# Optimization experiments

Measured on AMD Instinct MI355X. Metric: run time of the kernel, lower is better.

Reference implementation:

```python
import jax, jax.numpy as jnp
import numpy as np

N, F_IN, F_OUT, HEADS = 4096, 128, 64, 4


def setup_inputs() -> dict:
    key = jax.random.key(0)
    k1, k2, k3, k4, k5 = jax.random.split(key, 5)
    X = jax.random.normal(k1, (N, F_IN), dtype=jnp.float32)
    A = jax.random.randint(k2, (N, N), 0, 2, dtype=jnp.int32)
    # zero the diagonal: the torch loop always prepends the self node, so the
    # adjacency must not also contain it (would duplicate the self term).
    A = A * (1 - jnp.eye(N, dtype=jnp.int32))
    # per-head Linear(F_IN, F_OUT) weights/bias and Linear(2*F_OUT, 1, bias=False)
    W = jax.random.normal(k3, (HEADS, F_OUT, F_IN), dtype=jnp.float32) / np.sqrt(F_IN)
    b = jax.random.normal(k4, (HEADS, F_OUT), dtype=jnp.float32) * 0.02
    att = jax.random.normal(k5, (HEADS, 2 * F_OUT), dtype=jnp.float32) / np.sqrt(2 * F_OUT)
    return {"X": X, "A": A, "W": W, "b": b, "att": att}


def reference(X, A, W, b, att):
    # H[h, n, o] = line_h(X)
    H = jnp.einsum('nf,hof->hno', X, W) + b[:, None, :]
    f_out = W.shape[1]
    a_src, a_dst = att[:, :f_out], att[:, f_out:]
    # score e_ij = leaky_relu(a_src.H_i + a_dst.H_j)
    s = jnp.einsum('hno,ho->hn', H, a_src)  # query-side term (xi_bar expanded)
    d = jnp.einsum('hno,ho->hn', H, a_dst)  # neighbor-side term
    e = jax.nn.leaky_relu(s[:, :, None] + d[:, None, :])  # [H, N, N]
    # neighbor set = {self} U {j : A_ij != 0}
    mask = (A > 0) | jnp.eye(A.shape[0], dtype=bool)
    e = jnp.where(mask[None], e, -jnp.inf)
    alpha = jax.nn.softmax(e, axis=-1)  # segment softmax per node row
    # weighted sum per head, then mean over heads (sum / head in the original)
    out = jnp.einsum('hnm,hmo->no', alpha, H) / W.shape[0]
    return out  # [N, F_OUT]
```

## Files before the change

kernel.cpp:

```cpp
#include <hip/hip_runtime.h>
#include <hip/hip_bf16.h>


#define NN 4096
#define FIN 128
#define FOUT 64
#define NH 4

typedef __attribute__((ext_vector_type(8))) short bf16x8;
typedef __attribute__((ext_vector_type(4))) float f32x4;
typedef __attribute__((ext_vector_type(4))) unsigned int u32x4;

__device__ __forceinline__ unsigned short f32_bf16(float f) {
    unsigned u = __builtin_bit_cast(unsigned, f);
    u += 0x7fffu + ((u >> 16) & 1u);
    return (unsigned short)(u >> 16);
}

__device__ __forceinline__ void gload16(const void* g, void* l) {
    __builtin_amdgcn_global_load_lds(
        (const __attribute__((address_space(1))) unsigned*)g,
        (__attribute__((address_space(3))) unsigned*)l, 16, 0, 0);
}

__global__ __launch_bounds__(256) void pack_bits(
    const int* __restrict__ A, unsigned long long* __restrict__ Abits)
{
    const int row  = blockIdx.x;
    const int lane = threadIdx.x & 63;
    const int wv   = threadIdx.x >> 6;
    const int* arow = A + (size_t)row * NN;
    #pragma unroll 4
    for (int c = 0; c < 16; ++c) {
        const int col = c * 256 + wv * 64 + lane;
        unsigned long long m = __ballot(__builtin_nontemporal_load(&arow[col]) > 0);
        if (lane == 0) Abits[(size_t)row * 64 + c * 4 + wv] = m;
    }
}

__global__ __launch_bounds__(256) void gat_prep(
    const float* __restrict__ X, const float* __restrict__ W,
    const float* __restrict__ b, const float* __restrict__ att,
    unsigned short* __restrict__ HbfT, float* __restrict__ Hrow,
    float* __restrict__ s_out, float* __restrict__ d_out,
    float* __restrict__ es_g, float* __restrict__ es2_g,
    float* __restrict__ ed_g, float* __restrict__ ed2_g)
{
    const int rb = blockIdx.x;
    const int h  = blockIdx.y;
    const int n0 = rb * 32;
    const int t  = threadIdx.x;

    __shared__ float Xl[32][132];
    __shared__ float Wt[128][68];

    for (int g = t; g < 32 * 32; g += 256) {
        int row = g >> 5, c4 = g & 31;
        float4 v = *(const float4*)&X[(size_t)(n0 + row) * FIN + c4 * 4];
        *(float4*)&Xl[row][c4 * 4] = v;
    }
    for (int g = t; g < 64 * 32; g += 256) {
        int o = g >> 5, c4 = g & 31;
        float4 v = *(const float4*)&W[((size_t)h * FOUT + o) * FIN + c4 * 4];
        Wt[c4 * 4 + 0][o] = v.x; Wt[c4 * 4 + 1][o] = v.y;
        Wt[c4 * 4 + 2][o] = v.z; Wt[c4 * 4 + 3][o] = v.w;
    }
    __syncthreads();

    const int rg = t >> 4;
    const int og = t & 15;
    float acc[2][4] = {};

    #pragma unroll 4
    for (int f4 = 0; f4 < 32; ++f4) {
        float xv[2][4], wv[4][4];
        #pragma unroll
        for (int i = 0; i < 2; ++i) {
            float4 tmp = *(const float4*)&Xl[rg * 2 + i][f4 * 4];
            xv[i][0] = tmp.x; xv[i][1] = tmp.y; xv[i][2] = tmp.z; xv[i][3] = tmp.w;
        }
        #pragma unroll
        for (int k = 0; k < 4; ++k) {
            float4 tmp = *(const float4*)&Wt[f4 * 4 + k][og * 4];
            wv[k][0] = tmp.x; wv[k][1] = tmp.y; wv[k][2] = tmp.z; wv[k][3] = tmp.w;
        }
        #pragma unroll
        for (int i = 0; i < 2; ++i)
            #pragma unroll
            for (int k = 0; k < 4; ++k)
                #pragma unroll
                for (int jj = 0; jj < 4; ++jj)
                    acc[i][jj] = fmaf(xv[i][k], wv[k][jj], acc[i][jj]);
    }

    float bb[4], as_[4], ad_[4];
    #pragma unroll
    for (int jj = 0; jj < 4; ++jj) {
        bb[jj]  = b[h * FOUT + og * 4 + jj];
        as_[jj] = att[h * 2 * FOUT + og * 4 + jj];
        ad_[jj] = att[h * 2 * FOUT + FOUT + og * 4 + jj];
    }
    #pragma unroll
    for (int i = 0; i < 2; ++i)
        #pragma unroll
        for (int jj = 0; jj < 4; ++jj)
            acc[i][jj] += bb[jj];

    float sp[2] = {0.f, 0.f}, dp[2] = {0.f, 0.f};
    #pragma unroll
    for (int i = 0; i < 2; ++i)
        #pragma unroll
        for (int jj = 0; jj < 4; ++jj) {
            sp[i] = fmaf(acc[i][jj], as_[jj], sp[i]);
            dp[i] = fmaf(acc[i][jj], ad_[jj], dp[i]);
        }
    #pragma unroll
    for (int off = 1; off < 16; off <<= 1) {
        #pragma unroll
        for (int i = 0; i < 2; ++i) {
            sp[i] += __shfl_xor(sp[i], off);
            dp[i] += __shfl_xor(dp[i], off);
        }
    }
    if (og == 0) {
        #pragma unroll
        for (int i = 0; i < 2; ++i) {
            int nn = n0 + rg * 2 + i;
            s_out[h * NN + nn]  = sp[i];
            d_out[h * NN + nn]  = dp[i];
            es_g [h * NN + nn]  = __expf(sp[i]);
            es2_g[h * NN + nn]  = __expf(0.01f * sp[i]);
            ed_g [h * NN + nn]  = __expf(dp[i]);
            ed2_g[h * NN + nn]  = __expf(0.01f * dp[i]);
        }
    }

    #pragma unroll
    for (int i = 0; i < 2; ++i) {
        float4 v = make_float4(acc[i][0], acc[i][1], acc[i][2], acc[i][3]);
        *(float4*)&Hrow[((size_t)h * NN + n0 + rg * 2 + i) * FOUT + og * 4] = v;
    }
    #pragma unroll
    for (int jj = 0; jj < 4; ++jj) {
        int o = og * 4 + jj;
        ushort2 p;
        p.x = f32_bf16(acc[0][jj]);
        p.y = f32_bf16(acc[1][jj]);
        *(ushort2*)&HbfT[((size_t)h * FOUT + o) * NN + n0 + rg * 2] = p;
    }
}

struct SMem {
    union {
        __align__(16) unsigned short H[2][64][256];
        struct {
            float red[7][2][16][68];
            float redl[7][2][16];
        } fin;
    };
    unsigned bits[2][32][8];
    float ed [2][256];
    float ed2[2][256];
};

__global__ __launch_bounds__(1024, 8) void gat_main(
    const unsigned* __restrict__ Abits, const unsigned short* __restrict__ HbfT,
    const float* __restrict__ s_g, const float* __restrict__ d_g,
    const float* __restrict__ es_g, const float* __restrict__ es2_g,
    const float* __restrict__ ed_g, const float* __restrict__ ed2_g,
    const float* __restrict__ Hrow, float* __restrict__ outH)
{
    const int id   = blockIdx.x;
    const int h    = id & 3;
    const int tile = id >> 2;
    const int n0   = tile * 32;
    const int tid  = threadIdx.x;
    const int w    = tid >> 6;
    const int lane = tid & 63;
    const int r    = lane & 15;
    const int q    = lane >> 4;
    const int qs   = q * 8;
    const int rg   = w & 1;
    const int kg   = w >> 1;

    __shared__ SMem sm;

    const int nrow = n0 + rg * 16 + r;
    const float es  = es_g [h * NN + nrow];
    const float es2 = es2_g[h * NN + nrow];

    const int cb   = kg * 4 + q;
    const int sblk = (((cb & 15) ^ r) | (cb & 16));

    const int rowA = 4 * w + (lane >> 5);
    const int rowB = rowA + 2;
    const int blk  = lane & 31;
    const int gbA  = (((blk & 15) ^ (rowA & 15)) | (blk & 16));
    const int gbB  = (((blk & 15) ^ (rowB & 15)) | (blk & 16));
    const unsigned short* gHA = HbfT + ((size_t)(h * FOUT) + rowA) * NN + gbA * 8;
    const unsigned short* gHB = HbfT + ((size_t)(h * FOUT) + rowB) * NN + gbB * 8;
    const unsigned* gBits = Abits + (size_t)(n0 + (lane >> 1)) * 128 + (lane & 1) * 4;
    const float* gEd  = ed_g  + (size_t)h * NN + lane * 4;
    const float* gEd2 = ed2_g + (size_t)h * NN + lane * 4;

    bf16x8 ones;
    #pragma unroll
    for (int i = 0; i < 8; ++i) ones[i] = (short)0x3F80;

    f32x4 acc0 = {0,0,0,0}, acc1 = {0,0,0,0}, acc2 = {0,0,0,0},
          acc3 = {0,0,0,0}, accl = {0,0,0,0};

    gload16(gHA, &sm.H[0][4 * w][0]);
    gload16(gHB, &sm.H[0][4 * w + 2][0]);
    if      (w == 0) gload16(gBits, &sm.bits[0][0][0]);
    else if (w == 1) gload16(gEd,   &sm.ed [0][0]);
    else if (w == 2) gload16(gEd2,  &sm.ed2[0][0]);
    __syncthreads();

    #pragma unroll 2
    for (int ch = 0; ch < 16; ++ch) {
        const int buf = ch & 1;

        if (ch < 15) {
            const int nb = buf ^ 1;
            gload16(gHA + (ch + 1) * 256, &sm.H[nb][4 * w][0]);
            gload16(gHB + (ch + 1) * 256, &sm.H[nb][4 * w + 2][0]);
            if      (w == 0) gload16(gBits + (ch + 1) * 8,   &sm.bits[nb][0][0]);
            else if (w == 1) gload16(gEd   + (ch + 1) * 256, &sm.ed [nb][0]);
            else if (w == 2) gload16(gEd2  + (ch + 1) * 256, &sm.ed2[nb][0]);
        }

        const unsigned bits8 = sm.bits[buf][rg * 16 + r][kg] >> qs;
        const float4 e0 = *(const float4*)&sm.ed [buf][kg * 32 + qs];
        const float4 e1 = *(const float4*)&sm.ed [buf][kg * 32 + qs + 4];
        const float4 g0 = *(const float4*)&sm.ed2[buf][kg * 32 + qs];
        const float4 g1 = *(const float4*)&sm.ed2[buf][kg * 32 + qs + 4];
        const float edv [8] = {e0.x, e0.y, e0.z, e0.w, e1.x, e1.y, e1.z, e1.w};
        const float ed2v[8] = {g0.x, g0.y, g0.z, g0.w, g1.x, g1.y, g1.z, g1.w};

        u32x4 afu;
        #pragma unroll
        for (int p = 0; p < 4; ++p) {
            const int j0 = 2 * p, j1 = 2 * p + 1;
            float wa = (bits8 & (1u << j0))
                     ? fmaxf(es * edv[j0], es2 * ed2v[j0]) : 0.0f;
            float wb = (bits8 & (1u << j1))
                     ? fmaxf(es * edv[j1], es2 * ed2v[j1]) : 0.0f;
            __hip_bfloat162 pk = __float22bfloat162_rn(make_float2(wa, wb));
            unsigned u;
            __builtin_memcpy(&u, &pk, sizeof(u));
            afu[p] = u;
        }
        const bf16x8 af = __builtin_bit_cast(bf16x8, afu);

        const bf16x8 b0 = *(const bf16x8*)&sm.H[buf][r     ][sblk * 8];
        const bf16x8 b1 = *(const bf16x8*)&sm.H[buf][r + 16][sblk * 8];
        const bf16x8 b2 = *(const bf16x8*)&sm.H[buf][r + 32][sblk * 8];
        const bf16x8 b3 = *(const bf16x8*)&sm.H[buf][r + 48][sblk * 8];

        acc0 = __builtin_amdgcn_mfma_f32_16x16x32_bf16(af, b0,   acc0, 0, 0, 0);
        acc1 = __builtin_amdgcn_mfma_f32_16x16x32_bf16(af, b1,   acc1, 0, 0, 0);
        acc2 = __builtin_amdgcn_mfma_f32_16x16x32_bf16(af, b2,   acc2, 0, 0, 0);
        acc3 = __builtin_amdgcn_mfma_f32_16x16x32_bf16(af, b3,   acc3, 0, 0, 0);
        accl = __builtin_amdgcn_mfma_f32_16x16x32_bf16(af, ones, accl, 0, 0, 0);

        __syncthreads();
    }

    if (kg > 0) {
        #pragma unroll
        for (int reg = 0; reg < 4; ++reg) {
            const int rr = q * 4 + reg;
            sm.fin.red[kg - 1][rg][rr][ 0 + r] = acc0[reg];
            sm.fin.red[kg - 1][rg][rr][16 + r] = acc1[reg];
            sm.fin.red[kg - 1][rg][rr][32 + r] = acc2[reg];
            sm.fin.red[kg - 1][rg][rr][48 + r] = acc3[reg];
        }
        if (r == 0) {
            #pragma unroll
            for (int reg = 0; reg < 4; ++reg)
                sm.fin.redl[kg - 1][rg][q * 4 + reg] = accl[reg];
        }
    }
    __syncthreads();
    if (kg == 0) {
        #pragma unroll
        for (int kk = 0; kk < 7; ++kk) {
            #pragma unroll
            for (int reg = 0; reg < 4; ++reg) {
                const int rr = q * 4 + reg;
                acc0[reg] += sm.fin.red[kk][rg][rr][ 0 + r];
                acc1[reg] += sm.fin.red[kk][rg][rr][16 + r];
                acc2[reg] += sm.fin.red[kk][rg][rr][32 + r];
                acc3[reg] += sm.fin.red[kk][rg][rr][48 + r];
                accl[reg] += sm.fin.redl[kk][rg][rr];
            }
        }
        #pragma unroll
        for (int reg = 0; reg < 4; ++reg) {
            const int rr  = q * 4 + reg;
            const int nn2 = n0 + rg * 16 + rr;
            const float tt = s_g[h * NN + nn2] + d_g[h * NN + nn2];
            const float wd = __expf(fmaxf(tt, 0.01f * tt));
            const float inv = 0.25f / (accl[reg] + wd);
            const float* hr = &Hrow[((size_t)h * NN + nn2) * FOUT];
            float*       ob = &outH[((size_t)h * NN + nn2) * FOUT];
            ob[ 0 + r] = (acc0[reg] + wd * hr[ 0 + r]) * inv;
            ob[16 + r] = (acc1[reg] + wd * hr[16 + r]) * inv;
            ob[32 + r] = (acc2[reg] + wd * hr[32 + r]) * inv;
            ob[48 + r] = (acc3[reg] + wd * hr[48 + r]) * inv;
        }
    }
}

__global__ __launch_bounds__(256) void gat_fin(
    const float* __restrict__ outH, float* __restrict__ out)
{
    const int i = blockIdx.x * 256 + threadIdx.x;
    const f32x4* p = (const f32x4*)outH;
    f32x4 v0 = __builtin_nontemporal_load(p + i);
    f32x4 v1 = __builtin_nontemporal_load(p + i +  65536);
    f32x4 v2 = __builtin_nontemporal_load(p + i + 131072);
    f32x4 v3 = __builtin_nontemporal_load(p + i + 196608);
    f32x4 s = (v0 + v1) + (v2 + v3);
    *((f32x4*)out + i) = s;
}

extern "C" void kernel_launch(void* const* d_in, const int* in_sizes, int n_in,
                              void* d_out, int out_size, void* d_ws, size_t ws_size,
                              hipStream_t stream) {
    const float* X   = (const float*)d_in[0];
    const int*   A   = (const int*)  d_in[1];
    const float* W   = (const float*)d_in[2];
    const float* b   = (const float*)d_in[3];
    const float* att = (const float*)d_in[4];
    float* out = (float*)d_out;

    char* ws = (char*)d_ws;
    unsigned short* HbfT = (unsigned short*)ws;
    size_t off = (size_t)NH * FOUT * NN * 2;
    float* s_buf   = (float*)(ws + off);  off += (size_t)NH * NN * 4;
    float* d_buf   = (float*)(ws + off);  off += (size_t)NH * NN * 4;
    float* es_buf  = (float*)(ws + off);  off += (size_t)NH * NN * 4;
    float* es2_buf = (float*)(ws + off);  off += (size_t)NH * NN * 4;
    float* ed_buf  = (float*)(ws + off);  off += (size_t)NH * NN * 4;
    float* ed2_buf = (float*)(ws + off);  off += (size_t)NH * NN * 4;
    unsigned long long* Abits = (unsigned long long*)(ws + off);
    off += (size_t)NN * 64 * 8;
    float* Hrow   = (float*)(ws + off);
    off += (size_t)NH * NN * FOUT * 4;
    float* outH   = (float*)(ws + off);
    off += (size_t)NH * NN * FOUT * 4;

    pack_bits<<<NN, 256, 0, stream>>>(A, Abits);
    gat_prep<<<dim3(128, 4), 256, 0, stream>>>(X, W, b, att, HbfT, Hrow,
                                               s_buf, d_buf,
                                               es_buf, es2_buf, ed_buf, ed2_buf);
    gat_main<<<512, 1024, 0, stream>>>((const unsigned*)Abits, HbfT,
                                       s_buf, d_buf,
                                       es_buf, es2_buf, ed_buf, ed2_buf,
                                       Hrow, outH);
    gat_fin<<<256, 256, 0, stream>>>(outH, out);
}
```

Measured before the change: 172.2 us.

## Halve gat_main block to 512 threads, each wave covering two K sub-chunks

Shrinks the main aggregation block from 16 to 8 waves. Each wave now processes two 32-column slices of every 256-column chunk and issues four H tile loads instead of two. The cross-wave reduction shrinks from 7 partial buffers per row group to 3, and fewer waves share each barrier. In exchange, each wave carries more serial MFMA work per chunk, and there are fewer resident waves to hide the async load latency.

```diff
diff --git a/kernel.cpp b/kernel.cpp
--- a/kernel.cpp
+++ b/kernel.cpp
@@ -154,8 +154,8 @@
     union {
         __align__(16) unsigned short H[2][64][256];
         struct {
-            float red[7][2][16][68];
-            float redl[7][2][16];
+            float red[6][16][68];
+            float redl[6][16];
         } fin;
     };
     unsigned bits[2][32][8];
@@ -163,7 +163,7 @@
     float ed2[2][256];
 };
 
-__global__ __launch_bounds__(1024, 8) void gat_main(
+__global__ __launch_bounds__(512, 4) void gat_main(
     const unsigned* __restrict__ Abits, const unsigned short* __restrict__ HbfT,
     const float* __restrict__ s_g, const float* __restrict__ d_g,
     const float* __restrict__ es_g, const float* __restrict__ es2_g,
@@ -189,16 +189,16 @@
     const float es  = es_g [h * NN + nrow];
     const float es2 = es2_g[h * NN + nrow];
 
-    const int cb   = kg * 4 + q;
-    const int sblk = (((cb & 15) ^ r) | (cb & 16));
-
-    const int rowA = 4 * w + (lane >> 5);
-    const int rowB = rowA + 2;
-    const int blk  = lane & 31;
-    const int gbA  = (((blk & 15) ^ (rowA & 15)) | (blk & 16));
-    const int gbB  = (((blk & 15) ^ (rowB & 15)) | (blk & 16));
-    const unsigned short* gHA = HbfT + ((size_t)(h * FOUT) + rowA) * NN + gbA * 8;
-    const unsigned short* gHB = HbfT + ((size_t)(h * FOUT) + rowB) * NN + gbB * 8;
+    const int bb = ((kg * 4 + q) ^ r) & 15;
+
+    const int blk = lane & 31;
+    const unsigned short* gH[4];
+    #pragma unroll
+    for (int i = 0; i < 4; ++i) {
+        const int row = 8 * w + 2 * i + (lane >> 5);
+        const int gb  = ((blk & 15) ^ (row & 15)) | (blk & 16);
+        gH[i] = HbfT + ((size_t)(h * FOUT) + row) * NN + gb * 8;
+    }
     const unsigned* gBits = Abits + (size_t)(n0 + (lane >> 1)) * 128 + (lane & 1) * 4;
     const float* gEd  = ed_g  + (size_t)h * NN + lane * 4;
     const float* gEd2 = ed2_g + (size_t)h * NN + lane * 4;
@@ -210,11 +210,16 @@
     f32x4 acc0 = {0,0,0,0}, acc1 = {0,0,0,0}, acc2 = {0,0,0,0},
           acc3 = {0,0,0,0}, accl = {0,0,0,0};
 
-    gload16(gHA, &sm.H[0][4 * w][0]);
-    gload16(gHB, &sm.H[0][4 * w + 2][0]);
-    if      (w == 0) gload16(gBits, &sm.bits[0][0][0]);
-    else if (w == 1) gload16(gEd,   &sm.ed [0][0]);
-    else if (w == 2) gload16(gEd2,  &sm.ed2[0][0]);
+    {
+        unsigned short* hw = &sm.H[0][8 * w][0];
+        gload16(gH[0], hw);
+        gload16(gH[1], hw +  512);
+        gload16(gH[2], hw + 1024);
+        gload16(gH[3], hw + 1536);
+        if      (w == 0) gload16(gBits, &sm.bits[0][0][0]);
+        else if (w == 1) gload16(gEd,   &sm.ed [0][0]);
+        else if (w == 2) gload16(gEd2,  &sm.ed2[0][0]);
+    }
     __syncthreads();
 
     #pragma unroll 2
@@ -222,78 +227,120 @@
         const int buf = ch & 1;
 
         if (ch < 15) {
-            const int nb = buf ^ 1;
-            gload16(gHA + (ch + 1) * 256, &sm.H[nb][4 * w][0]);
-            gload16(gHB + (ch + 1) * 256, &sm.H[nb][4 * w + 2][0]);
-            if      (w == 0) gload16(gBits + (ch + 1) * 8,   &sm.bits[nb][0][0]);
-            else if (w == 1) gload16(gEd   + (ch + 1) * 256, &sm.ed [nb][0]);
-            else if (w == 2) gload16(gEd2  + (ch + 1) * 256, &sm.ed2[nb][0]);
-        }
-
-        const unsigned bits8 = sm.bits[buf][rg * 16 + r][kg] >> qs;
-        const float4 e0 = *(const float4*)&sm.ed [buf][kg * 32 + qs];
-        const float4 e1 = *(const float4*)&sm.ed [buf][kg * 32 + qs + 4];
-        const float4 g0 = *(const float4*)&sm.ed2[buf][kg * 32 + qs];
-        const float4 g1 = *(const float4*)&sm.ed2[buf][kg * 32 + qs + 4];
-        const float edv [8] = {e0.x, e0.y, e0.z, e0.w, e1.x, e1.y, e1.z, e1.w};
-        const float ed2v[8] = {g0.x, g0.y, g0.z, g0.w, g1.x, g1.y, g1.z, g1.w};
-
-        u32x4 afu;
-        #pragma unroll
-        for (int p = 0; p < 4; ++p) {
-            const int j0 = 2 * p, j1 = 2 * p + 1;
-            float wa = (bits8 & (1u << j0))
-                     ? fmaxf(es * edv[j0], es2 * ed2v[j0]) : 0.0f;
-            float wb = (bits8 & (1u << j1))
-                     ? fmaxf(es * edv[j1], es2 * ed2v[j1]) : 0.0f;
-            __hip_bfloat162 pk = __float22bfloat162_rn(make_float2(wa, wb));
-            unsigned u;
-            __builtin_memcpy(&u, &pk, sizeof(u));
-            afu[p] = u;
-        }
-        const bf16x8 af = __builtin_bit_cast(bf16x8, afu);
-
-        const bf16x8 b0 = *(const bf16x8*)&sm.H[buf][r     ][sblk * 8];
-        const bf16x8 b1 = *(const bf16x8*)&sm.H[buf][r + 16][sblk * 8];
-        const bf16x8 b2 = *(const bf16x8*)&sm.H[buf][r + 32][sblk * 8];
-        const bf16x8 b3 = *(const bf16x8*)&sm.H[buf][r + 48][sblk * 8];
-
-        acc0 = __builtin_amdgcn_mfma_f32_16x16x32_bf16(af, b0,   acc0, 0, 0, 0);
-        acc1 = __builtin_amdgcn_mfma_f32_16x16x32_bf16(af, b1,   acc1, 0, 0, 0);
-        acc2 = __builtin_amdgcn_mfma_f32_16x16x32_bf16(af, b2,   acc2, 0, 0, 0);
-        acc3 = __builtin_amdgcn_mfma_f32_16x16x32_bf16(af, b3,   acc3, 0, 0, 0);
-        accl = __builtin_amdgcn_mfma_f32_16x16x32_bf16(af, ones, accl, 0, 0, 0);
+            const int nb   = buf ^ 1;
+            const int coff = (ch + 1) * 256;
+            unsigned short* hw = &sm.H[nb][8 * w][0];
+            gload16(gH[0] + coff, hw);
+            gload16(gH[1] + coff, hw +  512);
+            gload16(gH[2] + coff, hw + 1024);
+            gload16(gH[3] + coff, hw + 1536);
+            if      (w == 0) gload16(gBits + (ch + 1) * 8, &sm.bits[nb][0][0]);
+            else if (w == 1) gload16(gEd  + coff, &sm.ed [nb][0]);
+            else if (w == 2) gload16(gEd2 + coff, &sm.ed2[nb][0]);
+        }
+
+        {
+            const unsigned bits8 = sm.bits[buf][rg * 16 + r][kg] >> qs;
+            const float4 e0 = *(const float4*)&sm.ed [buf][kg * 32 + qs];
+            const float4 e1 = *(const float4*)&sm.ed [buf][kg * 32 + qs + 4];
+            const float4 g0 = *(const float4*)&sm.ed2[buf][kg * 32 + qs];
+            const float4 g1 = *(const float4*)&sm.ed2[buf][kg * 32 + qs + 4];
+            const float edv [8] = {e0.x, e0.y, e0.z, e0.w, e1.x, e1.y, e1.z, e1.w};
+            const float ed2v[8] = {g0.x, g0.y, g0.z, g0.w, g1.x, g1.y, g1.z, g1.w};
+            u32x4 afu;
+            #pragma unroll
+            for (int p = 0; p < 4; ++p) {
+                const int j0 = 2 * p, j1 = 2 * p + 1;
+                float wa = (bits8 & (1u << j0))
+                         ? fmaxf(es * edv[j0], es2 * ed2v[j0]) : 0.0f;
+                float wb = (bits8 & (1u << j1))
+                         ? fmaxf(es * edv[j1], es2 * ed2v[j1]) : 0.0f;
+                __hip_bfloat162 pk = __float22bfloat162_rn(make_float2(wa, wb));
+                unsigned u;
+                __builtin_memcpy(&u, &pk, sizeof(u));
+                afu[p] = u;
+            }
+            const bf16x8 af = __builtin_bit_cast(bf16x8, afu);
+
+            const bf16x8 b0 = *(const bf16x8*)&sm.H[buf][r     ][bb * 8];
+            const bf16x8 b1 = *(const bf16x8*)&sm.H[buf][r + 16][bb * 8];
+            const bf16x8 b2 = *(const bf16x8*)&sm.H[buf][r + 32][bb * 8];
+            const bf16x8 b3 = *(const bf16x8*)&sm.H[buf][r + 48][bb * 8];
+
+            acc0 = __builtin_amdgcn_mfma_f32_16x16x32_bf16(af, b0,   acc0, 0, 0, 0);
+            acc1 = __builtin_amdgcn_mfma_f32_16x16x32_bf16(af, b1,   acc1, 0, 0, 0);
+            acc2 = __builtin_amdgcn_mfma_f32_16x16x32_bf16(af, b2,   acc2, 0, 0, 0);
+            acc3 = __builtin_amdgcn_mfma_f32_16x16x32_bf16(af, b3,   acc3, 0, 0, 0);
+            accl = __builtin_amdgcn_mfma_f32_16x16x32_bf16(af, ones, accl, 0, 0, 0);
+        }
+
+        {
+            const unsigned bits8 = sm.bits[buf][rg * 16 + r][kg + 4] >> qs;
+            const float4 e0 = *(const float4*)&sm.ed [buf][128 + kg * 32 + qs];
+            const float4 e1 = *(const float4*)&sm.ed [buf][128 + kg * 32 + qs + 4];
+            const float4 g0 = *(const float4*)&sm.ed2[buf][128 + kg * 32 + qs];
+            const float4 g1 = *(const float4*)&sm.ed2[buf][128 + kg * 32 + qs + 4];
+            const float edv [8] = {e0.x, e0.y, e0.z, e0.w, e1.x, e1.y, e1.z, e1.w};
+            const float ed2v[8] = {g0.x, g0.y, g0.z, g0.w, g1.x, g1.y, g1.z, g1.w};
+            u32x4 afu;
+            #pragma unroll
+            for (int p = 0; p < 4; ++p) {
+                const int j0 = 2 * p, j1 = 2 * p + 1;
+                float wa = (bits8 & (1u << j0))
+                         ? fmaxf(es * edv[j0], es2 * ed2v[j0]) : 0.0f;
+                float wb = (bits8 & (1u << j1))
+                         ? fmaxf(es * edv[j1], es2 * ed2v[j1]) : 0.0f;
+                __hip_bfloat162 pk = __float22bfloat162_rn(make_float2(wa, wb));
+                unsigned u;
+                __builtin_memcpy(&u, &pk, sizeof(u));
+                afu[p] = u;
+            }
+            const bf16x8 af = __builtin_bit_cast(bf16x8, afu);
+
+            const bf16x8 b0 = *(const bf16x8*)&sm.H[buf][r     ][128 + bb * 8];
+            const bf16x8 b1 = *(const bf16x8*)&sm.H[buf][r + 16][128 + bb * 8];
+            const bf16x8 b2 = *(const bf16x8*)&sm.H[buf][r + 32][128 + bb * 8];
+            const bf16x8 b3 = *(const bf16x8*)&sm.H[buf][r + 48][128 + bb * 8];
+
+            acc0 = __builtin_amdgcn_mfma_f32_16x16x32_bf16(af, b0,   acc0, 0, 0, 0);
+            acc1 = __builtin_amdgcn_mfma_f32_16x16x32_bf16(af, b1,   acc1, 0, 0, 0);
+            acc2 = __builtin_amdgcn_mfma_f32_16x16x32_bf16(af, b2,   acc2, 0, 0, 0);
+            acc3 = __builtin_amdgcn_mfma_f32_16x16x32_bf16(af, b3,   acc3, 0, 0, 0);
+            accl = __builtin_amdgcn_mfma_f32_16x16x32_bf16(af, ones, accl, 0, 0, 0);
+        }
 
         __syncthreads();
     }
 
     if (kg > 0) {
+        const int widx = (kg - 1) * 2 + rg;
         #pragma unroll
         for (int reg = 0; reg < 4; ++reg) {
             const int rr = q * 4 + reg;
-            sm.fin.red[kg - 1][rg][rr][ 0 + r] = acc0[reg];
-            sm.fin.red[kg - 1][rg][rr][16 + r] = acc1[reg];
-            sm.fin.red[kg - 1][rg][rr][32 + r] = acc2[reg];
-            sm.fin.red[kg - 1][rg][rr][48 + r] = acc3[reg];
+            sm.fin.red[widx][rr][ 0 + r] = acc0[reg];
+            sm.fin.red[widx][rr][16 + r] = acc1[reg];
+            sm.fin.red[widx][rr][32 + r] = acc2[reg];
+            sm.fin.red[widx][rr][48 + r] = acc3[reg];
         }
         if (r == 0) {
             #pragma unroll
             for (int reg = 0; reg < 4; ++reg)
-                sm.fin.redl[kg - 1][rg][q * 4 + reg] = accl[reg];
+                sm.fin.redl[widx][q * 4 + reg] = accl[reg];
         }
     }
     __syncthreads();
     if (kg == 0) {
         #pragma unroll
-        for (int kk = 0; kk < 7; ++kk) {
+        for (int kk = 0; kk < 3; ++kk) {
+            const int widx = kk * 2 + rg;
             #pragma unroll
             for (int reg = 0; reg < 4; ++reg) {
                 const int rr = q * 4 + reg;
-                acc0[reg] += sm.fin.red[kk][rg][rr][ 0 + r];
-                acc1[reg] += sm.fin.red[kk][rg][rr][16 + r];
-                acc2[reg] += sm.fin.red[kk][rg][rr][32 + r];
-                acc3[reg] += sm.fin.red[kk][rg][rr][48 + r];
-                accl[reg] += sm.fin.redl[kk][rg][rr];
+                acc0[reg] += sm.fin.red[widx][rr][ 0 + r];
+                acc1[reg] += sm.fin.red[widx][rr][16 + r];
+                acc2[reg] += sm.fin.red[widx][rr][32 + r];
+                acc3[reg] += sm.fin.red[widx][rr][48 + r];
+                accl[reg] += sm.fin.redl[widx][rr];
             }
         }
         #pragma unroll
@@ -356,9 +403,9 @@
     gat_prep<<<dim3(128, 4), 256, 0, stream>>>(X, W, b, att, HbfT, Hrow,
                                                s_buf, d_buf,
                                                es_buf, es2_buf, ed_buf, ed2_buf);
-    gat_main<<<512, 1024, 0, stream>>>((const unsigned*)Abits, HbfT,
-                                       s_buf, d_buf,
-                                       es_buf, es2_buf, ed_buf, ed2_buf,
-                                       Hrow, outH);
+    gat_main<<<512, 512, 0, stream>>>((const unsigned*)Abits, HbfT,
+                                      s_buf, d_buf,
+                                      es_buf, es2_buf, ed_buf, ed2_buf,
+                                      Hrow, outH);
     gat_fin<<<256, 256, 0, stream>>>(outH, out);
 }
```

Result: faster. 157.6 us (-8.4%).
